# Kernel tuning notes

Hardware: AMD Instinct MI355X
Metric: run time of the kernel (lower is better)

The kernel has to match this reference:

```python
import jax, jax.numpy as jnp
import numpy as np

N_CELLS = 100000
IN_CH = 64
N_EDGES = 1280000


def setup_inputs() -> dict:
    key = jax.random.key(0)
    k1, k2, k3, k4, k5 = jax.random.split(key, 5)
    x_source = jax.random.normal(k1, (N_CELLS, IN_CH), dtype=jnp.float32)
    att_weight = jax.random.normal(k2, (2 * IN_CH,), dtype=jnp.float32)
    nbhd_values = jax.random.uniform(k3, (N_EDGES,), dtype=jnp.float32)
    target_index_i = jnp.sort(jax.random.randint(k4, (N_EDGES,), 0, N_CELLS))
    source_index_j = jax.random.randint(k5, (N_EDGES,), 0, N_CELLS)
    return {
        "x_source": x_source,
        "att_weight": att_weight,
        "nbhd_values": nbhd_values,
        "target_index_i": target_index_i,
        "source_index_j": source_index_j,
    }


def reference(x_source, att_weight, nbhd_values, target_index_i, source_index_j):
    # gather per-message endpoint features: [E, C] each
    x_src_msg = x_source[source_index_j]
    x_tgt_msg = x_source[target_index_i]  # x_target is None -> use x_source
    # attention: elu(cat([src, tgt]) @ w) -> [E]
    att = jax.nn.elu(
        jnp.concatenate([x_src_msg, x_tgt_msg], axis=1) @ att_weight
    )
    # modulate sparse neighborhood values by attention, scale messages
    vals = nbhd_values * att  # [E]
    x_message = vals[:, None] * x_src_msg  # [E, C]
    # scatter-sum into target cells: [N, C]
    return jax.ops.segment_sum(x_message, target_index_i, num_segments=N_CELLS)
```

## Files before the change

kernel.cpp:

```cpp
#include <hip/hip_runtime.h>

#define N_CELLS 100000
#define IN_CH 64
#define N_EDGES 1280000
#define MAXW 4

__device__ __forceinline__ unsigned short f32_to_bf16(float f) {
    unsigned u = __float_as_uint(f);
    u += 0x7FFFu + ((u >> 16) & 1u);
    return (unsigned short)(u >> 16);
}
__device__ __forceinline__ float bf16_to_f32(unsigned short h) {
    return __uint_as_float((unsigned)h << 16);
}

__global__ void __launch_bounds__(256) score_kernel(
    const float* __restrict__ x, const float* __restrict__ w,
    float* __restrict__ s_src, float* __restrict__ s_tgt,
    unsigned short* __restrict__ xb, int n_cells) {
    int gid  = blockIdx.x * 256 + threadIdx.x;
    int wave = gid >> 6;
    int lane = threadIdx.x & 63;
    int grp  = lane >> 4;
    int sub  = lane & 15;
    int cell = wave * 4 + grp;

    float4 xv = make_float4(0.f, 0.f, 0.f, 0.f);
    if (cell < n_cells)
        xv = *(const float4*)&x[(((unsigned)cell << 6) | ((unsigned)sub << 2))];
    if (xb && cell < n_cells) {
        ushort4 hb;
        hb.x = f32_to_bf16(xv.x); hb.y = f32_to_bf16(xv.y);
        hb.z = f32_to_bf16(xv.z); hb.w = f32_to_bf16(xv.w);
        *(ushort4*)&xb[(((unsigned)cell << 6) | ((unsigned)sub << 2))] = hb;
    }
    const float4* w4 = (const float4*)w;
    float4 wa = w4[sub];
    float4 wb = w4[16 + sub];
    float a = xv.x * wa.x + xv.y * wa.y + xv.z * wa.z + xv.w * wa.w;
    float b = xv.x * wb.x + xv.y * wb.y + xv.z * wb.z + xv.w * wb.w;
#pragma unroll
    for (int off = 8; off; off >>= 1) {
        a += __shfl_xor(a, off, 64);
        b += __shfl_xor(b, off, 64);
    }
    if (sub == 0 && cell < n_cells) {
        s_src[cell] = a;
        s_tgt[cell] = b;
    }
}

__global__ void __launch_bounds__(256) edge_kernel(
    const int* __restrict__ tgt, const int* __restrict__ src,
    const float* __restrict__ nbhd,
    const float* __restrict__ s_src, const float* __restrict__ s_tgt,
    int* __restrict__ row_start, float* __restrict__ vals,
    int n_edges, int n_cells) {
    int e = blockIdx.x * 256 + threadIdx.x;
    if (e >= n_edges) return;
    int lane = threadIdx.x & 63;
    int t = tgt[e];
    float a = s_src[src[e]] + s_tgt[t];
    vals[e] = nbhd[e] * (a > 0.f ? a : expm1f(a));
    int prev = __shfl_up(t, 1, 64);
    if (lane == 0) prev = (e == 0) ? -1 : tgt[e - 1];
    for (int c = prev + 1; c <= t; ++c) row_start[c] = e;
    if (e == n_edges - 1) {
        for (int c = t + 1; c <= n_cells; ++c) row_start[c] = n_edges;
    }
}

__global__ void __launch_bounds__(256) agg_kernel(
    const unsigned short* __restrict__ xb, const int* __restrict__ src,
    const float* __restrict__ vals, const int* __restrict__ row_start,
    float* __restrict__ out, int n_cells) {
    int gid  = blockIdx.x * 256 + threadIdx.x;
    int lane = threadIdx.x & 63;
    int grp  = lane >> 4;
    int sub  = lane & 15;
    int cell = (gid >> 6) * 4 + grp;
    unsigned suboff = (unsigned)sub << 2;
    int gbase = grp << 4;

    int lo  = row_start[cell];
    int hi  = row_start[cell + 1];
    int cnt = hi - lo;
    int cntP = cnt > (MAXW * 16) ? (MAXW * 16) : cnt;

    int   jr[MAXW];
    float vr[MAXW];
#pragma unroll
    for (int c = 0; c < MAXW; ++c) {
        int t16 = (c << 4) + sub;
        int j = 0; float v = 0.f;
        if (t16 < cntP) {
            int idx = lo + t16;
            j = src[idx];
            v = vals[idx];
        }
        jr[c] = j; vr[c] = v;
    }

    float4 acc = make_float4(0.f, 0.f, 0.f, 0.f);
#pragma unroll
    for (int c = 0; c < MAXW; ++c) {
        int wc = cntP - (c << 4);
        if (wc <= 0) break;
        if (wc > 16) wc = 16;
        int t = 0;
        for (; t + 8 <= wc; t += 8) {
#pragma unroll
            for (int u = 0; u < 8; u += 4) {
                int   j0 = __shfl(jr[c], gbase + t + u,     64);
                int   j1 = __shfl(jr[c], gbase + t + u + 1, 64);
                int   j2 = __shfl(jr[c], gbase + t + u + 2, 64);
                int   j3 = __shfl(jr[c], gbase + t + u + 3, 64);
                float v0 = __shfl(vr[c], gbase + t + u,     64);
                float v1 = __shfl(vr[c], gbase + t + u + 1, 64);
                float v2 = __shfl(vr[c], gbase + t + u + 2, 64);
                float v3 = __shfl(vr[c], gbase + t + u + 3, 64);
                ushort4 h0 = *(const ushort4*)&xb[(((unsigned)j0 << 6) | suboff)];
                ushort4 h1 = *(const ushort4*)&xb[(((unsigned)j1 << 6) | suboff)];
                ushort4 h2 = *(const ushort4*)&xb[(((unsigned)j2 << 6) | suboff)];
                ushort4 h3 = *(const ushort4*)&xb[(((unsigned)j3 << 6) | suboff)];
                acc.x = fmaf(v0, bf16_to_f32(h0.x), acc.x);
                acc.y = fmaf(v0, bf16_to_f32(h0.y), acc.y);
                acc.z = fmaf(v0, bf16_to_f32(h0.z), acc.z);
                acc.w = fmaf(v0, bf16_to_f32(h0.w), acc.w);
                acc.x = fmaf(v1, bf16_to_f32(h1.x), acc.x);
                acc.y = fmaf(v1, bf16_to_f32(h1.y), acc.y);
                acc.z = fmaf(v1, bf16_to_f32(h1.z), acc.z);
                acc.w = fmaf(v1, bf16_to_f32(h1.w), acc.w);
                acc.x = fmaf(v2, bf16_to_f32(h2.x), acc.x);
                acc.y = fmaf(v2, bf16_to_f32(h2.y), acc.y);
                acc.z = fmaf(v2, bf16_to_f32(h2.z), acc.z);
                acc.w = fmaf(v2, bf16_to_f32(h2.w), acc.w);
                acc.x = fmaf(v3, bf16_to_f32(h3.x), acc.x);
                acc.y = fmaf(v3, bf16_to_f32(h3.y), acc.y);
                acc.z = fmaf(v3, bf16_to_f32(h3.z), acc.z);
                acc.w = fmaf(v3, bf16_to_f32(h3.w), acc.w);
            }
        }
        for (; t + 4 <= wc; t += 4) {
            int   j0 = __shfl(jr[c], gbase + t,     64);
            int   j1 = __shfl(jr[c], gbase + t + 1, 64);
            int   j2 = __shfl(jr[c], gbase + t + 2, 64);
            int   j3 = __shfl(jr[c], gbase + t + 3, 64);
            float v0 = __shfl(vr[c], gbase + t,     64);
            float v1 = __shfl(vr[c], gbase + t + 1, 64);
            float v2 = __shfl(vr[c], gbase + t + 2, 64);
            float v3 = __shfl(vr[c], gbase + t + 3, 64);
            ushort4 h0 = *(const ushort4*)&xb[(((unsigned)j0 << 6) | suboff)];
            ushort4 h1 = *(const ushort4*)&xb[(((unsigned)j1 << 6) | suboff)];
            ushort4 h2 = *(const ushort4*)&xb[(((unsigned)j2 << 6) | suboff)];
            ushort4 h3 = *(const ushort4*)&xb[(((unsigned)j3 << 6) | suboff)];
            acc.x = fmaf(v0, bf16_to_f32(h0.x), acc.x);
            acc.y = fmaf(v0, bf16_to_f32(h0.y), acc.y);
            acc.z = fmaf(v0, bf16_to_f32(h0.z), acc.z);
            acc.w = fmaf(v0, bf16_to_f32(h0.w), acc.w);
            acc.x = fmaf(v1, bf16_to_f32(h1.x), acc.x);
            acc.y = fmaf(v1, bf16_to_f32(h1.y), acc.y);
            acc.z = fmaf(v1, bf16_to_f32(h1.z), acc.z);
            acc.w = fmaf(v1, bf16_to_f32(h1.w), acc.w);
            acc.x = fmaf(v2, bf16_to_f32(h2.x), acc.x);
            acc.y = fmaf(v2, bf16_to_f32(h2.y), acc.y);
            acc.z = fmaf(v2, bf16_to_f32(h2.z), acc.z);
            acc.w = fmaf(v2, bf16_to_f32(h2.w), acc.w);
            acc.x = fmaf(v3, bf16_to_f32(h3.x), acc.x);
            acc.y = fmaf(v3, bf16_to_f32(h3.y), acc.y);
            acc.z = fmaf(v3, bf16_to_f32(h3.z), acc.z);
            acc.w = fmaf(v3, bf16_to_f32(h3.w), acc.w);
        }
        for (; t < wc; ++t) {
            int   jt = __shfl(jr[c], gbase + t, 64);
            float vt = __shfl(vr[c], gbase + t, 64);
            ushort4 h = *(const ushort4*)&xb[(((unsigned)jt << 6) | suboff)];
            acc.x = fmaf(vt, bf16_to_f32(h.x), acc.x);
            acc.y = fmaf(vt, bf16_to_f32(h.y), acc.y);
            acc.z = fmaf(vt, bf16_to_f32(h.z), acc.z);
            acc.w = fmaf(vt, bf16_to_f32(h.w), acc.w);
        }
    }

    for (int base = lo + MAXW * 16; base < hi; base += 16) {
        int cc = hi - base;
        if (cc > 16) cc = 16;
        int   j = 0;
        float v = 0.f;
        if (sub < cc) {
            j = src[base + sub];
            v = vals[base + sub];
        }
        for (int t = 0; t < cc; ++t) {
            int   jt = __shfl(j, gbase + t, 64);
            float vt = __shfl(v, gbase + t, 64);
            ushort4 h = *(const ushort4*)&xb[(((unsigned)jt << 6) | suboff)];
            acc.x = fmaf(vt, bf16_to_f32(h.x), acc.x);
            acc.y = fmaf(vt, bf16_to_f32(h.y), acc.y);
            acc.z = fmaf(vt, bf16_to_f32(h.z), acc.z);
            acc.w = fmaf(vt, bf16_to_f32(h.w), acc.w);
        }
    }

    *(float4*)&out[(((unsigned)cell << 6) | suboff)] = acc;
}

__global__ void __launch_bounds__(256) agg_kernel_f32(
    const float* __restrict__ x, const int* __restrict__ src,
    const float* __restrict__ nbhd,
    const float* __restrict__ s_src, const float* __restrict__ s_tgt,
    const int* __restrict__ row_start,
    float* __restrict__ out, int n_cells) {
    int gid  = blockIdx.x * 256 + threadIdx.x;
    int lane = threadIdx.x & 63;
    int grp  = lane >> 4;
    int sub  = lane & 15;
    int cell = (gid >> 6) * 4 + grp;
    unsigned suboff = (unsigned)sub << 2;
    int gbase = grp << 4;

    int lo = 0, hi = 0;
    float sti = 0.f;
    if (cell < n_cells) {
        lo  = row_start[cell];
        hi  = row_start[cell + 1];
        sti = s_tgt[cell];
    }
    float4 acc = make_float4(0.f, 0.f, 0.f, 0.f);
    for (int base = lo; base < hi; base += 16) {
        int cc = hi - base;
        if (cc > 16) cc = 16;
        int   j = 0;
        float v = 0.f;
        if (sub < cc) {
            j = src[base + sub];
            float a = s_src[j] + sti;
            v = nbhd[base + sub] * (a > 0.f ? a : expm1f(a));
        }
        for (int t = 0; t < cc; ++t) {
            int   jt = __shfl(j, gbase + t, 64);
            float vt = __shfl(v, gbase + t, 64);
            float4 xt = *(const float4*)&x[(((unsigned)jt << 6) | suboff)];
            acc.x = fmaf(vt, xt.x, acc.x); acc.y = fmaf(vt, xt.y, acc.y);
            acc.z = fmaf(vt, xt.z, acc.z); acc.w = fmaf(vt, xt.w, acc.w);
        }
    }
    if (cell < n_cells)
        *(float4*)&out[(((unsigned)cell << 6) | suboff)] = acc;
}

extern "C" void kernel_launch(void* const* d_in, const int* in_sizes, int n_in,
                              void* d_out, int out_size, void* d_ws, size_t ws_size,
                              hipStream_t stream) {
    const float* x    = (const float*)d_in[0];
    const float* w    = (const float*)d_in[1];
    const float* nbhd = (const float*)d_in[2];
    const int*   tgt  = (const int*)d_in[3];
    const int*   src  = (const int*)d_in[4];
    float*       out  = (float*)d_out;

    float* s_src     = (float*)d_ws;
    float* s_tgt     = s_src + N_CELLS;
    int*   row_start = (int*)(s_tgt + N_CELLS);
    float* vals      = (float*)(row_start + N_CELLS + 1);
    unsigned short* xb = (unsigned short*)(vals + N_EDGES);
    size_t need_full = (size_t)(3 * N_CELLS + 1 + N_EDGES) * 4
                     + (size_t)N_CELLS * IN_CH * 2;
    bool full = ws_size >= need_full;

    int sblocks = (N_CELLS * 16 + 255) / 256;
    int eblocks = (N_EDGES + 255) / 256;

    if (full) {
        score_kernel<<<sblocks, 256, 0, stream>>>(x, w, s_src, s_tgt, xb, N_CELLS);
        edge_kernel<<<eblocks, 256, 0, stream>>>(tgt, src, nbhd, s_src, s_tgt,
                                                 row_start, vals, N_EDGES, N_CELLS);
        int ablocks = (N_CELLS * 16) / 256;
        agg_kernel<<<ablocks, 256, 0, stream>>>(xb, src, vals, row_start, out, N_CELLS);
    } else {
        score_kernel<<<sblocks, 256, 0, stream>>>(x, w, s_src, s_tgt,
                                                  (unsigned short*)nullptr, N_CELLS);
        edge_kernel<<<eblocks, 256, 0, stream>>>(tgt, src, nbhd, s_src, s_tgt,
                                                 row_start, vals, N_EDGES, N_CELLS);
        int ablocks = (N_CELLS * 16 + 255) / 256;
        agg_kernel_f32<<<ablocks, 256, 0, stream>>>(x, src, nbhd, s_src, s_tgt,
                                                    row_start, out, N_CELLS);
    }
}
```

Before: 64.71 us.

## Merge score and row-start kernels, compute edge attention inside aggregation

Fuses the per-cell score kernel and the row-start construction into one launch, using disjoint block ranges for each, since the row-start work no longer depends on the scores. The per-edge attention value is now computed inside the aggregation kernel from s_src, s_tgt and nbhd instead of being written to and read back from a separate vals buffer. This removes one kernel launch and a round trip of the edge-sized intermediate through memory, at the cost of an extra dependent s_src gather in the aggregation prologue. It also swaps expm1f for __expf(a)-1, which loses some precision for small negative inputs.

```diff
diff --git a/kernel.cpp b/kernel.cpp
--- a/kernel.cpp
+++ b/kernel.cpp
@@ -13,66 +13,69 @@
 __device__ __forceinline__ float bf16_to_f32(unsigned short h) {
     return __uint_as_float((unsigned)h << 16);
 }
-
-__global__ void __launch_bounds__(256) score_kernel(
+__device__ __forceinline__ float elu_fast(float a) {
+    return a > 0.f ? a : (__expf(a) - 1.f);
+}
+
+#define SCORE_BLOCKS ((N_CELLS * 16 + 255) / 256)
+#define ROWSTART_BLOCKS ((N_EDGES + 255) / 256)
+
+__global__ void __launch_bounds__(256) prep_kernel(
     const float* __restrict__ x, const float* __restrict__ w,
+    const int* __restrict__ tgt,
     float* __restrict__ s_src, float* __restrict__ s_tgt,
-    unsigned short* __restrict__ xb, int n_cells) {
-    int gid  = blockIdx.x * 256 + threadIdx.x;
-    int wave = gid >> 6;
-    int lane = threadIdx.x & 63;
-    int grp  = lane >> 4;
-    int sub  = lane & 15;
-    int cell = wave * 4 + grp;
-
-    float4 xv = make_float4(0.f, 0.f, 0.f, 0.f);
-    if (cell < n_cells)
-        xv = *(const float4*)&x[(((unsigned)cell << 6) | ((unsigned)sub << 2))];
-    if (xb && cell < n_cells) {
-        ushort4 hb;
-        hb.x = f32_to_bf16(xv.x); hb.y = f32_to_bf16(xv.y);
-        hb.z = f32_to_bf16(xv.z); hb.w = f32_to_bf16(xv.w);
-        *(ushort4*)&xb[(((unsigned)cell << 6) | ((unsigned)sub << 2))] = hb;
-    }
-    const float4* w4 = (const float4*)w;
-    float4 wa = w4[sub];
-    float4 wb = w4[16 + sub];
-    float a = xv.x * wa.x + xv.y * wa.y + xv.z * wa.z + xv.w * wa.w;
-    float b = xv.x * wb.x + xv.y * wb.y + xv.z * wb.z + xv.w * wb.w;
-#pragma unroll
-    for (int off = 8; off; off >>= 1) {
-        a += __shfl_xor(a, off, 64);
-        b += __shfl_xor(b, off, 64);
-    }
-    if (sub == 0 && cell < n_cells) {
-        s_src[cell] = a;
-        s_tgt[cell] = b;
-    }
-}
-
-__global__ void __launch_bounds__(256) edge_kernel(
-    const int* __restrict__ tgt, const int* __restrict__ src,
+    unsigned short* __restrict__ xb, int* __restrict__ row_start,
+    int n_cells, int n_edges) {
+    if (blockIdx.x < SCORE_BLOCKS) {
+        int gid  = blockIdx.x * 256 + threadIdx.x;
+        int wave = gid >> 6;
+        int lane = threadIdx.x & 63;
+        int grp  = lane >> 4;
+        int sub  = lane & 15;
+        int cell = wave * 4 + grp;
+
+        float4 xv = make_float4(0.f, 0.f, 0.f, 0.f);
+        if (cell < n_cells)
+            xv = *(const float4*)&x[(((unsigned)cell << 6) | ((unsigned)sub << 2))];
+        if (xb && cell < n_cells) {
+            ushort4 hb;
+            hb.x = f32_to_bf16(xv.x); hb.y = f32_to_bf16(xv.y);
+            hb.z = f32_to_bf16(xv.z); hb.w = f32_to_bf16(xv.w);
+            *(ushort4*)&xb[(((unsigned)cell << 6) | ((unsigned)sub << 2))] = hb;
+        }
+        const float4* w4 = (const float4*)w;
+        float4 wa = w4[sub];
+        float4 wb = w4[16 + sub];
+        float a = xv.x * wa.x + xv.y * wa.y + xv.z * wa.z + xv.w * wa.w;
+        float b = xv.x * wb.x + xv.y * wb.y + xv.z * wb.z + xv.w * wb.w;
+#pragma unroll
+        for (int off = 8; off; off >>= 1) {
+            a += __shfl_xor(a, off, 64);
+            b += __shfl_xor(b, off, 64);
+        }
+        if (sub == 0 && cell < n_cells) {
+            s_src[cell] = a;
+            s_tgt[cell] = b;
+        }
+    } else {
+        int e = (blockIdx.x - SCORE_BLOCKS) * 256 + threadIdx.x;
+        if (e >= n_edges) return;
+        int lane = threadIdx.x & 63;
+        int t = tgt[e];
+        int prev = __shfl_up(t, 1, 64);
+        if (lane == 0) prev = (e == 0) ? -1 : tgt[e - 1];
+        for (int c = prev + 1; c <= t; ++c) row_start[c] = e;
+        if (e == n_edges - 1) {
+            for (int c = t + 1; c <= n_cells; ++c) row_start[c] = n_edges;
+        }
+    }
+}
+
+__global__ void __launch_bounds__(256) agg_kernel(
+    const unsigned short* __restrict__ xb, const int* __restrict__ src,
     const float* __restrict__ nbhd,
     const float* __restrict__ s_src, const float* __restrict__ s_tgt,
-    int* __restrict__ row_start, float* __restrict__ vals,
-    int n_edges, int n_cells) {
-    int e = blockIdx.x * 256 + threadIdx.x;
-    if (e >= n_edges) return;
-    int lane = threadIdx.x & 63;
-    int t = tgt[e];
-    float a = s_src[src[e]] + s_tgt[t];
-    vals[e] = nbhd[e] * (a > 0.f ? a : expm1f(a));
-    int prev = __shfl_up(t, 1, 64);
-    if (lane == 0) prev = (e == 0) ? -1 : tgt[e - 1];
-    for (int c = prev + 1; c <= t; ++c) row_start[c] = e;
-    if (e == n_edges - 1) {
-        for (int c = t + 1; c <= n_cells; ++c) row_start[c] = n_edges;
-    }
-}
-
-__global__ void __launch_bounds__(256) agg_kernel(
-    const unsigned short* __restrict__ xb, const int* __restrict__ src,
-    const float* __restrict__ vals, const int* __restrict__ row_start,
+    const int* __restrict__ row_start,
     float* __restrict__ out, int n_cells) {
     int gid  = blockIdx.x * 256 + threadIdx.x;
     int lane = threadIdx.x & 63;
@@ -84,22 +87,31 @@
 
     int lo  = row_start[cell];
     int hi  = row_start[cell + 1];
-    int cnt = hi - lo;
+    float sti = s_tgt[cell];
+    int cnt  = hi - lo;
     int cntP = cnt > (MAXW * 16) ? (MAXW * 16) : cnt;
 
     int   jr[MAXW];
-    float vr[MAXW];
+    float nr[MAXW];
 #pragma unroll
     for (int c = 0; c < MAXW; ++c) {
         int t16 = (c << 4) + sub;
-        int j = 0; float v = 0.f;
+        int j = 0; float n = 0.f;
         if (t16 < cntP) {
             int idx = lo + t16;
             j = src[idx];
-            v = vals[idx];
-        }
-        jr[c] = j; vr[c] = v;
-    }
+            n = nbhd[idx];
+        }
+        jr[c] = j; nr[c] = n;
+    }
+    float sr[MAXW];
+#pragma unroll
+    for (int c = 0; c < MAXW; ++c)
+        sr[c] = s_src[jr[c]];
+    float vr[MAXW];
+#pragma unroll
+    for (int c = 0; c < MAXW; ++c)
+        vr[c] = nr[c] * elu_fast(sr[c] + sti);
 
     float4 acc = make_float4(0.f, 0.f, 0.f, 0.f);
 #pragma unroll
@@ -189,7 +201,7 @@
         float v = 0.f;
         if (sub < cc) {
             j = src[base + sub];
-            v = vals[base + sub];
+            v = nbhd[base + sub] * elu_fast(s_src[j] + sti);
         }
         for (int t = 0; t < cc; ++t) {
             int   jt = __shfl(j, gbase + t, 64);
@@ -234,8 +246,7 @@
         float v = 0.f;
         if (sub < cc) {
             j = src[base + sub];
-            float a = s_src[j] + sti;
-            v = nbhd[base + sub] * (a > 0.f ? a : expm1f(a));
+            v = nbhd[base + sub] * elu_fast(s_src[j] + sti);
         }
         for (int t = 0; t < cc; ++t) {
             int   jt = __shfl(j, gbase + t, 64);
@@ -262,26 +273,21 @@
     float* s_src     = (float*)d_ws;
     float* s_tgt     = s_src + N_CELLS;
     int*   row_start = (int*)(s_tgt + N_CELLS);
-    float* vals      = (float*)(row_start + N_CELLS + 1);
-    unsigned short* xb = (unsigned short*)(vals + N_EDGES);
-    size_t need_full = (size_t)(3 * N_CELLS + 1 + N_EDGES) * 4
-                     + (size_t)N_CELLS * IN_CH * 2;
+    unsigned short* xb = (unsigned short*)(row_start + N_CELLS + 1);
+    size_t need_full = (size_t)(3 * N_CELLS + 1) * 4 + (size_t)N_CELLS * IN_CH * 2;
     bool full = ws_size >= need_full;
 
-    int sblocks = (N_CELLS * 16 + 255) / 256;
-    int eblocks = (N_EDGES + 255) / 256;
-
+    {
+        int blocks = SCORE_BLOCKS + ROWSTART_BLOCKS;
+        prep_kernel<<<blocks, 256, 0, stream>>>(x, w, tgt, s_src, s_tgt,
+                                                full ? xb : (unsigned short*)nullptr,
+                                                row_start, N_CELLS, N_EDGES);
+    }
     if (full) {
-        score_kernel<<<sblocks, 256, 0, stream>>>(x, w, s_src, s_tgt, xb, N_CELLS);
-        edge_kernel<<<eblocks, 256, 0, stream>>>(tgt, src, nbhd, s_src, s_tgt,
-                                                 row_start, vals, N_EDGES, N_CELLS);
         int ablocks = (N_CELLS * 16) / 256;
-        agg_kernel<<<ablocks, 256, 0, stream>>>(xb, src, vals, row_start, out, N_CELLS);
+        agg_kernel<<<ablocks, 256, 0, stream>>>(xb, src, nbhd, s_src, s_tgt,
+                                                row_start, out, N_CELLS);
     } else {
-        score_kernel<<<sblocks, 256, 0, stream>>>(x, w, s_src, s_tgt,
-                                                  (unsigned short*)nullptr, N_CELLS);
-        edge_kernel<<<eblocks, 256, 0, stream>>>(tgt, src, nbhd, s_src, s_tgt,
-                                                 row_start, vals, N_EDGES, N_CELLS);
         int ablocks = (N_CELLS * 16 + 255) / 256;
         agg_kernel_f32<<<ablocks, 256, 0, stream>>>(x, src, nbhd, s_src, s_tgt,
                                                     row_start, out, N_CELLS);
```

After: 59.72 us. 7.7% less time.
